# Optimization experiments

Measured on AMD Instinct MI355X. Metric: run time of the kernel, lower is better.

Reference implementation:

```python
import jax, jax.numpy as jnp
import numpy as np

K_PATCHES = 25
GRID_SIDE = 20            # sqrt(10000 // 25)
G = GRID_SIDE * GRID_SIDE # 400 points per patch
LATENT = 1024
DIMS = [LATENT + 2, 1024, 512, 256, 128, 3]  # per-layer in/out channels
BATCH = 16


def setup_inputs() -> dict:
    key = jax.random.key(0)
    ks = jax.random.split(key, 11)
    x = jax.random.normal(ks[0], (BATCH, LATENT), dtype=jnp.float32)
    params = {}
    # PyTorch Conv1d default init: U(-1/sqrt(fan_in), 1/sqrt(fan_in)); one weight set per patch.
    for i in range(5):
        fan_in = DIMS[i]
        bound = 1.0 / np.sqrt(fan_in)
        params[f"W{i+1}"] = jax.random.uniform(
            ks[1 + 2 * i], (K_PATCHES, DIMS[i], DIMS[i + 1]), jnp.float32, -bound, bound)
        params[f"b{i+1}"] = jax.random.uniform(
            ks[2 + 2 * i], (K_PATCHES, DIMS[i + 1]), jnp.float32, -bound, bound)
    return {"x": x, **params}


def reference(x, W1, b1, W2, b2, W3, b3, W4, b4, W5, b5):
    B = x.shape[0]
    # Deterministic UV grid (random_grid=False): same 20x20 grid for every patch.
    g = jnp.linspace(0.0, 1.0, GRID_SIDE)
    X, Y = jnp.meshgrid(g, g, indexing='xy')
    grid = jnp.stack([X, Y], axis=-1).reshape(-1, 2)  # (G, 2)
    # Build per-patch features: latent broadcast to every point + 2 uv coords.
    lat = jnp.broadcast_to(x[:, None, None, :], (B, K_PATCHES, G, LATENT))
    uv = jnp.broadcast_to(grid[None, None], (B, K_PATCHES, G, 2))
    h = jnp.concatenate([lat, uv], axis=-1)  # (B, P, G, 1026)
    # 1x1 Conv1d == per-point linear; batched over patches via grouped einsum.
    for W, b in ((W1, b1), (W2, b2), (W3, b3), (W4, b4)):
        h = jax.nn.relu(jnp.einsum('bpgi,pio->bpgo', h, W) + b[None, :, None, :])
    out = jnp.tanh(jnp.einsum('bpgi,pio->bpgo', h, W5) + b5[None, :, None, :])
    return out  # (B, P, G, 3) == torch stack(dim=1).permute(0,1,3,2)
```

## Files before the change

### kernel.cpp

```cpp
#include <hip/hip_runtime.h>
#include <math.h>

#define K_PATCHES 25
#define GRID_SIDE 20
#define G_PTS     400
#define LATENT    1024
#define BATCH     16

typedef _Float16 f16x8 __attribute__((ext_vector_type(8)));
typedef _Float16 f16x4 __attribute__((ext_vector_type(4)));
typedef float    f32x4 __attribute__((ext_vector_type(4)));

#define BASE_OFF 0
#define WT2_OFF  1638400
#define WT3_OFF  27852800
#define WT4_OFF  34406400

__global__ __launch_bounds__(128)
void base_kernel(const float* __restrict__ x,
                 const float* __restrict__ W1,
                 const float* __restrict__ b1,
                 float* __restrict__ base) {
    __shared__ float xs[BATCH][LATENT];
    const int p  = blockIdx.x >> 3;
    const int oc = blockIdx.x & 7;
    const int o  = oc * 128 + threadIdx.x;

    for (int idx = threadIdx.x; idx < BATCH * LATENT / 4; idx += 128)
        ((float4*)xs)[idx] = ((const float4*)x)[idx];
    __syncthreads();

    float acc[BATCH];
#pragma unroll
    for (int b = 0; b < BATCH; ++b) acc[b] = 0.0f;

    const float* Wp = W1 + (size_t)p * 1026 * 1024 + o;
    for (int k = 0; k < LATENT; k += 4) {
        const float w0 = Wp[(size_t)(k + 0) * 1024];
        const float w1 = Wp[(size_t)(k + 1) * 1024];
        const float w2 = Wp[(size_t)(k + 2) * 1024];
        const float w3 = Wp[(size_t)(k + 3) * 1024];
#pragma unroll
        for (int b = 0; b < BATCH; ++b) {
            const float4 xv = *(const float4*)&xs[b][k];
            acc[b] = fmaf(xv.w, w3, fmaf(xv.z, w2, fmaf(xv.y, w1, fmaf(xv.x, w0, acc[b]))));
        }
    }

    const float bias = b1[p * 1024 + o];
    for (int b = 0; b < BATCH; ++b)
        base[(size_t)(b * K_PATCHES + p) * 1024 + o] = acc[b] + bias;
}

__global__ __launch_bounds__(256)
void conv_tr_kernel(const float* __restrict__ W, _Float16* __restrict__ Wt,
                    int K, int N) {
    __shared__ float tile[64][65];
    const int tpp = (K / 64) * (N / 64);
    const int p   = blockIdx.x / tpp;
    const int rem = blockIdx.x % tpp;
    const int kt  = rem / (N / 64);
    const int nt  = rem % (N / 64);
    const int tr  = threadIdx.x >> 6;
    const int tc  = threadIdx.x & 63;

    const float* Wp = W + ((size_t)p * K + kt * 64) * N + nt * 64;
#pragma unroll
    for (int i = 0; i < 64; i += 4)
        tile[i + tr][tc] = Wp[(size_t)(i + tr) * N + tc];
    __syncthreads();

    _Float16* Wtp = Wt + ((size_t)p * N + nt * 64) * K + kt * 64;
#pragma unroll
    for (int i = 0; i < 64; i += 4)
        Wtp[(size_t)(i + tr) * K + tc] = (_Float16)tile[tc][i + tr];
}

__global__ __launch_bounds__(512)
void fused_mfma(const float* __restrict__ base,
                const float* __restrict__ W1,
                const _Float16* __restrict__ Wt2, const float* __restrict__ b2,
                const _Float16* __restrict__ Wt3, const float* __restrict__ b3,
                const _Float16* __restrict__ Wt4, const float* __restrict__ b4,
                const float* __restrict__ W5, const float* __restrict__ b5,
                float* __restrict__ out) {
    __shared__ __align__(16) unsigned char LDS[139264];
    constexpr int OFF_SB = 0;
    constexpr int OFF_WU = 8192;
    constexpr int OFF_WV = 12288;
    constexpr int OFF_H1 = 16384;
    constexpr int OFF_H2 = 24576;
    constexpr int OFF_H3 = 90112;
    constexpr int OFF_H4 = 122880;

    const int bid = blockIdx.x;
    const int xcd = bid & 7;
    const int ii  = bid >> 3;
    const int ord = (xcd < 4) ? xcd * 313 + ii : 4 * 313 + (xcd - 4) * 312 + ii;
    const int p     = ord / 100;
    const int rbase = (ord % 100) * 64;

    const int t    = threadIdx.x;
    const int lane = t & 63;
    const int w    = t >> 6;
    const int l16  = lane & 15;
    const int lq   = lane >> 4;

    float* sb0  = (float*)(LDS + OFF_SB);
    float* sb1  = sb0 + 1024;
    float* swuf = (float*)(LDS + OFF_WU);
    float* swvf = (float*)(LDS + OFF_WV);

    const int b0  = rbase / 400;
    const int b1i = (rbase + 63) / 400;
    {
        const float* base0 = base + (size_t)(b0 * K_PATCHES + p) * 1024;
        const float* base1 = base + (size_t)(b1i * K_PATCHES + p) * 1024;
        const float* wup   = W1 + (size_t)p * 1026 * 1024 + (size_t)1024 * 1024;
        if (t < 256) ((float4*)sb0)[t] = ((const float4*)base0)[t];
        else         ((float4*)sb1)[t - 256] = ((const float4*)base1)[t - 256];
        if (t < 256) ((float4*)swuf)[t] = ((const float4*)wup)[t];
        else         ((float4*)swvf)[t - 256] = ((const float4*)(wup + 1024))[t - 256];
    }
    __syncthreads();

    const int pko   = t >> 7;
    const int pr    = (t >> 1) & 63;
    const int phalf = t & 1;
    const float* sbm2 = (rbase + pr < (b0 + 1) * 400) ? sb0 : sb1;
    const int pg  = (rbase + pr) % 400;
    const float pu = (float)(pg % GRID_SIDE) * (1.0f / 19.0f);
    const float pv = (float)(pg / GRID_SIDE) * (1.0f / 19.0f);
    const unsigned pwoff = (unsigned)((pko * 64 + pr) * 16 + phalf * 8);

    auto produce2 = [&](int kc, unsigned char* dst) {
        const int k = kc + pko * 8 + phalf * 4;
        const float4 bv = *(const float4*)&sbm2[k];
        const float4 uu = *(const float4*)&swuf[k];
        const float4 vv = *(const float4*)&swvf[k];
        f16x4 hv;
        hv[0] = (_Float16)fmaxf(fmaf(pv, vv.x, fmaf(pu, uu.x, bv.x)), 0.0f);
        hv[1] = (_Float16)fmaxf(fmaf(pv, vv.y, fmaf(pu, uu.y, bv.y)), 0.0f);
        hv[2] = (_Float16)fmaxf(fmaf(pv, vv.z, fmaf(pu, uu.z, bv.z)), 0.0f);
        hv[3] = (_Float16)fmaxf(fmaf(pv, vv.w, fmaf(pu, uu.w, bv.w)), 0.0f);
        *(f16x4*)(dst + pwoff) = hv;
    };

    const _Float16* Wt2p = Wt2 + (size_t)p * 512 * 1024;
    const _Float16* b2base = Wt2p + (size_t)(w * 64 + l16) * 1024 + lq * 8;
    f32x4 acc2[4][4];
    {
        const float* b2p = b2 + p * 512;
#pragma unroll
        for (int nf = 0; nf < 4; ++nf) {
            const float bias = b2p[w * 64 + nf * 16 + l16];
            f32x4 bv = {bias, bias, bias, bias};
#pragma unroll
            for (int mf = 0; mf < 4; ++mf) acc2[mf][nf] = bv;
        }
    }

    f16x8 bA[4], bB[4];
    produce2(0, LDS + OFF_H1);
#pragma unroll
    for (int nf = 0; nf < 4; ++nf)
        bA[nf] = *(const f16x8*)(b2base + (size_t)nf * 16384);
    __syncthreads();

    auto l2step = [&](int c, f16x8 (&bc)[4], f16x8 (&bn)[4]) {
        const unsigned char* h1b = LDS + OFF_H1 + (c & 1) * 4096;
        if (c < 31) {
            const int kc1 = (c + 1) * 32;
#pragma unroll
            for (int nf = 0; nf < 4; ++nf)
                bn[nf] = *(const f16x8*)(b2base + (size_t)nf * 16384 + kc1);
            produce2(kc1, LDS + OFF_H1 + ((c + 1) & 1) * 4096);
        }
        f16x8 a[4];
#pragma unroll
        for (int mf = 0; mf < 4; ++mf)
            a[mf] = *(const f16x8*)(h1b + (lq * 64 + mf * 16 + l16) * 16);
        __builtin_amdgcn_s_setprio(1);
#pragma unroll
        for (int mf = 0; mf < 4; ++mf)
#pragma unroll
            for (int nf = 0; nf < 4; ++nf)
                acc2[mf][nf] = __builtin_amdgcn_mfma_f32_16x16x32_f16(a[mf], bc[nf], acc2[mf][nf], 0, 0, 0);
        __builtin_amdgcn_s_setprio(0);
        __syncthreads();
    };

#pragma unroll 1
    for (int c = 0; c < 32; c += 2) {
        l2step(c,     bA, bB);
        l2step(c + 1, bB, bA);
    }

#pragma unroll
    for (int mf = 0; mf < 4; ++mf)
#pragma unroll
        for (int nf = 0; nf < 4; ++nf)
#pragma unroll
            for (int r = 0; r < 4; ++r) {
                const int row = mf * 16 + lq * 4 + r;
                const int col = w * 64 + nf * 16 + l16;
                const float v = fmaxf(acc2[mf][nf][r], 0.0f);
                *(_Float16*)(LDS + OFF_H2 + ((col >> 3) * 64 + row) * 16 + (col & 7) * 2) = (_Float16)v;
            }
    __syncthreads();

    const _Float16* Wt3p = Wt3 + (size_t)p * 256 * 512;
    const _Float16* b3base = Wt3p + (size_t)(w * 32 + l16) * 512 + lq * 8;
    f32x4 acc3[4][2];
    {
        const float* b3p = b3 + p * 256;
#pragma unroll
        for (int nf = 0; nf < 2; ++nf) {
            const float bias = b3p[w * 32 + nf * 16 + l16];
            f32x4 bv = {bias, bias, bias, bias};
#pragma unroll
            for (int mf = 0; mf < 4; ++mf) acc3[mf][nf] = bv;
        }
    }
    f16x8 cA[2], cB[2];
#pragma unroll
    for (int nf = 0; nf < 2; ++nf)
        cA[nf] = *(const f16x8*)(b3base + (size_t)nf * 8192);

    auto l3step = [&](int c, f16x8 (&bc)[2], f16x8 (&bn)[2]) {
        if (c < 15) {
            const int kc1 = (c + 1) * 32;
#pragma unroll
            for (int nf = 0; nf < 2; ++nf)
                bn[nf] = *(const f16x8*)(b3base + (size_t)nf * 8192 + kc1);
        }
        f16x8 a[4];
#pragma unroll
        for (int mf = 0; mf < 4; ++mf)
            a[mf] = *(const f16x8*)(LDS + OFF_H2 + ((c * 4 + lq) * 64 + mf * 16 + l16) * 16);
        __builtin_amdgcn_s_setprio(1);
#pragma unroll
        for (int mf = 0; mf < 4; ++mf)
#pragma unroll
            for (int nf = 0; nf < 2; ++nf)
                acc3[mf][nf] = __builtin_amdgcn_mfma_f32_16x16x32_f16(a[mf], bc[nf], acc3[mf][nf], 0, 0, 0);
        __builtin_amdgcn_s_setprio(0);
    };

#pragma unroll 1
    for (int c = 0; c < 16; c += 2) {
        l3step(c,     cA, cB);
        l3step(c + 1, cB, cA);
    }

#pragma unroll
    for (int mf = 0; mf < 4; ++mf)
#pragma unroll
        for (int nf = 0; nf < 2; ++nf)
#pragma unroll
            for (int r = 0; r < 4; ++r) {
                const int row = mf * 16 + lq * 4 + r;
                const int col = w * 32 + nf * 16 + l16;
                const float v = fmaxf(acc3[mf][nf][r], 0.0f);
                *(_Float16*)(LDS + OFF_H3 + ((col >> 3) * 64 + row) * 16 + (col & 7) * 2) = (_Float16)v;
            }
    __syncthreads();

    const _Float16* Wt4p = Wt4 + (size_t)p * 128 * 256;
    const _Float16* b4base = Wt4p + (size_t)(w * 16 + l16) * 256 + lq * 8;
    f32x4 acc4[4];
    {
        const float* b4p = b4 + p * 128;
        const float bias = b4p[w * 16 + l16];
        f32x4 bv = {bias, bias, bias, bias};
#pragma unroll
        for (int mf = 0; mf < 4; ++mf) acc4[mf] = bv;
    }
    f16x8 dA, dB;
    dA = *(const f16x8*)(b4base);

    auto l4step = [&](int c, f16x8& bc, f16x8& bn) {
        if (c < 7)
            bn = *(const f16x8*)(b4base + (c + 1) * 32);
        f16x8 a[4];
#pragma unroll
        for (int mf = 0; mf < 4; ++mf)
            a[mf] = *(const f16x8*)(LDS + OFF_H3 + ((c * 4 + lq) * 64 + mf * 16 + l16) * 16);
        __builtin_amdgcn_s_setprio(1);
#pragma unroll
        for (int mf = 0; mf < 4; ++mf)
            acc4[mf] = __builtin_amdgcn_mfma_f32_16x16x32_f16(a[mf], bc, acc4[mf], 0, 0, 0);
        __builtin_amdgcn_s_setprio(0);
    };

#pragma unroll 1
    for (int c = 0; c < 8; c += 2) {
        l4step(c,     dA, dB);
        l4step(c + 1, dB, dA);
    }

#pragma unroll
    for (int mf = 0; mf < 4; ++mf)
#pragma unroll
        for (int r = 0; r < 4; ++r) {
            const int row = mf * 16 + lq * 4 + r;
            const int col = w * 16 + l16;
            const float v = fmaxf(acc4[mf][r], 0.0f);
            *(_Float16*)(LDS + OFF_H4 + ((col >> 3) * 64 + row) * 16 + (col & 7) * 2) = (_Float16)v;
        }
    __syncthreads();

    if (t < 192) {
        const int m = t / 3;
        const int c = t % 3;
        const float* W5p = W5 + p * 128 * 3;
        float acc = b5[p * 3 + c];
#pragma unroll 4
        for (int k = 0; k < 128; ++k) {
            const _Float16 hv = *(const _Float16*)(LDS + OFF_H4 + ((k >> 3) * 64 + m) * 16 + (k & 7) * 2);
            acc = fmaf((float)hv, W5p[k * 3 + c], acc);
        }
        const int r  = rbase + m;
        const int bb = r / 400;
        const int gg = r % 400;
        out[((size_t)(bb * K_PATCHES + p) * G_PTS + gg) * 3 + c] = tanhf(acc);
    }
}

extern "C" void kernel_launch(void* const* d_in, const int* in_sizes, int n_in,
                              void* d_out, int out_size, void* d_ws, size_t ws_size,
                              hipStream_t stream) {
    const float* x  = (const float*)d_in[0];
    const float* W1 = (const float*)d_in[1];
    const float* b1 = (const float*)d_in[2];
    const float* W2 = (const float*)d_in[3];
    const float* b2 = (const float*)d_in[4];
    const float* W3 = (const float*)d_in[5];
    const float* b3 = (const float*)d_in[6];
    const float* W4 = (const float*)d_in[7];
    const float* b4 = (const float*)d_in[8];
    const float* W5 = (const float*)d_in[9];
    const float* b5 = (const float*)d_in[10];
    float* out = (float*)d_out;

    float*     base = (float*)((char*)d_ws + BASE_OFF);
    _Float16*  Wt2  = (_Float16*)((char*)d_ws + WT2_OFF);
    _Float16*  Wt3  = (_Float16*)((char*)d_ws + WT3_OFF);
    _Float16*  Wt4  = (_Float16*)((char*)d_ws + WT4_OFF);

    base_kernel<<<K_PATCHES * 8, 128, 0, stream>>>(x, W1, b1, base);

    conv_tr_kernel<<<K_PATCHES * (1024 / 64) * (512 / 64), 256, 0, stream>>>(W2, Wt2, 1024, 512);
    conv_tr_kernel<<<K_PATCHES * (512 / 64) * (256 / 64),  256, 0, stream>>>(W3, Wt3, 512, 256);
    conv_tr_kernel<<<K_PATCHES * (256 / 64) * (128 / 64),  256, 0, stream>>>(W4, Wt4, 256, 128);

    fused_mfma<<<K_PATCHES * 100, 512, 0, stream>>>(
        base, W1, Wt2, b2, Wt3, b3, Wt4, b4, W5, b5, out);
}
```

Before: 594.5 us.

## Split fused MLP kernel into two lower-LDS kernels via fp16 workspace intermediate

The single fused kernel used about 136 KB of LDS per block, which limited occupancy. It is split into gemm_l12 (layers 1-2, writes h2 as fp16 to global workspace) and gemm_l345 (layers 3-5, reads h2 straight from global into registers). Each uses far less LDS and sets launch_bounds occupancy hints. The three weight-transpose launches are also merged into one. This costs an extra roundtrip of about 164 MB of fp16 activations through memory, and the split path only runs when the workspace is large enough, otherwise it falls back to the fused kernel.

Result: slower. 720.6 us (+21.2%).

```diff
diff --git a/kernel.cpp b/kernel.cpp
--- a/kernel.cpp
+++ b/kernel.cpp
@@ -15,6 +15,8 @@
 #define WT2_OFF  1638400
 #define WT3_OFF  27852800
 #define WT4_OFF  34406400
+#define H2WS_OFF 36044800
+#define WS_NEED  (36044800ull + 163840000ull)
 
 __global__ __launch_bounds__(128)
 void base_kernel(const float* __restrict__ x,
@@ -53,12 +55,19 @@
 }
 
 __global__ __launch_bounds__(256)
-void conv_tr_kernel(const float* __restrict__ W, _Float16* __restrict__ Wt,
-                    int K, int N) {
+void conv_tr_all(const float* __restrict__ W2, _Float16* __restrict__ Wt2,
+                 const float* __restrict__ W3, _Float16* __restrict__ Wt3,
+                 const float* __restrict__ W4, _Float16* __restrict__ Wt4) {
     __shared__ float tile[64][65];
+    int bb = blockIdx.x;
+    const float* W; _Float16* Wt; int K, N, rel;
+    if (bb < 3200)      { W = W2; Wt = Wt2; K = 1024; N = 512; rel = bb; }
+    else if (bb < 4000) { W = W3; Wt = Wt3; K = 512;  N = 256; rel = bb - 3200; }
+    else                { W = W4; Wt = Wt4; K = 256;  N = 128; rel = bb - 4000; }
+
     const int tpp = (K / 64) * (N / 64);
-    const int p   = blockIdx.x / tpp;
-    const int rem = blockIdx.x % tpp;
+    const int p   = rel / tpp;
+    const int rem = rel % tpp;
     const int kt  = rem / (N / 64);
     const int nt  = rem % (N / 64);
     const int tr  = threadIdx.x >> 6;
@@ -74,6 +83,280 @@
 #pragma unroll
     for (int i = 0; i < 64; i += 4)
         Wtp[(size_t)(i + tr) * K + tc] = (_Float16)tile[tc][i + tr];
+}
+
+__device__ __forceinline__ int tile_ord(int bid) {
+    const int xcd = bid & 7;
+    const int ii  = bid >> 3;
+    return (xcd < 4) ? xcd * 313 + ii : 4 * 313 + (xcd - 4) * 312 + ii;
+}
+
+__global__ __launch_bounds__(512, 4)
+void gemm_l12(const float* __restrict__ base,
+              const float* __restrict__ W1,
+              const _Float16* __restrict__ Wt2, const float* __restrict__ b2,
+              _Float16* __restrict__ h2g) {
+    __shared__ __align__(16) unsigned char LDS[24576];
+    constexpr int OFF_SB = 0;
+    constexpr int OFF_WU = 8192;
+    constexpr int OFF_WV = 12288;
+    constexpr int OFF_H1 = 16384;
+
+    const int ord   = tile_ord(blockIdx.x);
+    const int p     = ord / 100;
+    const int rbase = (ord % 100) * 64;
+
+    const int t    = threadIdx.x;
+    const int lane = t & 63;
+    const int w    = t >> 6;
+    const int l16  = lane & 15;
+    const int lq   = lane >> 4;
+
+    float* sb0  = (float*)(LDS + OFF_SB);
+    float* sb1  = sb0 + 1024;
+    float* swuf = (float*)(LDS + OFF_WU);
+    float* swvf = (float*)(LDS + OFF_WV);
+
+    const int b0  = rbase / 400;
+    const int b1i = (rbase + 63) / 400;
+    {
+        const float* base0 = base + (size_t)(b0 * K_PATCHES + p) * 1024;
+        const float* base1 = base + (size_t)(b1i * K_PATCHES + p) * 1024;
+        const float* wup   = W1 + (size_t)p * 1026 * 1024 + (size_t)1024 * 1024;
+        if (t < 256) ((float4*)sb0)[t] = ((const float4*)base0)[t];
+        else         ((float4*)sb1)[t - 256] = ((const float4*)base1)[t - 256];
+        if (t < 256) ((float4*)swuf)[t] = ((const float4*)wup)[t];
+        else         ((float4*)swvf)[t - 256] = ((const float4*)(wup + 1024))[t - 256];
+    }
+    __syncthreads();
+
+    const int pko   = t >> 7;
+    const int pr    = (t >> 1) & 63;
+    const int phalf = t & 1;
+    const float* sbm2 = (rbase + pr < (b0 + 1) * 400) ? sb0 : sb1;
+    const int pg  = (rbase + pr) % 400;
+    const float pu = (float)(pg % GRID_SIDE) * (1.0f / 19.0f);
+    const float pv = (float)(pg / GRID_SIDE) * (1.0f / 19.0f);
+    const unsigned pwoff = (unsigned)((pko * 64 + pr) * 16 + phalf * 8);
+
+    auto produce2 = [&](int kc, unsigned char* dst) {
+        const int k = kc + pko * 8 + phalf * 4;
+        const float4 bv = *(const float4*)&sbm2[k];
+        const float4 uu = *(const float4*)&swuf[k];
+        const float4 vv = *(const float4*)&swvf[k];
+        f16x4 hv;
+        hv[0] = (_Float16)fmaxf(fmaf(pv, vv.x, fmaf(pu, uu.x, bv.x)), 0.0f);
+        hv[1] = (_Float16)fmaxf(fmaf(pv, vv.y, fmaf(pu, uu.y, bv.y)), 0.0f);
+        hv[2] = (_Float16)fmaxf(fmaf(pv, vv.z, fmaf(pu, uu.z, bv.z)), 0.0f);
+        hv[3] = (_Float16)fmaxf(fmaf(pv, vv.w, fmaf(pu, uu.w, bv.w)), 0.0f);
+        *(f16x4*)(dst + pwoff) = hv;
+    };
+
+    const _Float16* Wt2p = Wt2 + (size_t)p * 512 * 1024;
+    const _Float16* b2base = Wt2p + (size_t)(w * 64 + l16) * 1024 + lq * 8;
+    f32x4 acc2[4][4];
+    {
+        const float* b2p = b2 + p * 512;
+#pragma unroll
+        for (int nf = 0; nf < 4; ++nf) {
+            const float bias = b2p[w * 64 + nf * 16 + l16];
+            f32x4 bv = {bias, bias, bias, bias};
+#pragma unroll
+            for (int mf = 0; mf < 4; ++mf) acc2[mf][nf] = bv;
+        }
+    }
+
+    f16x8 bA[4], bB[4];
+    produce2(0, LDS + OFF_H1);
+#pragma unroll
+    for (int nf = 0; nf < 4; ++nf)
+        bA[nf] = *(const f16x8*)(b2base + (size_t)nf * 16384);
+    __syncthreads();
+
+    auto l2step = [&](int c, f16x8 (&bc)[4], f16x8 (&bn)[4]) {
+        const unsigned char* h1b = LDS + OFF_H1 + (c & 1) * 4096;
+        if (c < 31) {
+            const int kc1 = (c + 1) * 32;
+#pragma unroll
+            for (int nf = 0; nf < 4; ++nf)
+                bn[nf] = *(const f16x8*)(b2base + (size_t)nf * 16384 + kc1);
+            produce2(kc1, LDS + OFF_H1 + ((c + 1) & 1) * 4096);
+        }
+        f16x8 a[4];
+#pragma unroll
+        for (int mf = 0; mf < 4; ++mf)
+            a[mf] = *(const f16x8*)(h1b + (lq * 64 + mf * 16 + l16) * 16);
+        __builtin_amdgcn_s_setprio(1);
+#pragma unroll
+        for (int mf = 0; mf < 4; ++mf)
+#pragma unroll
+            for (int nf = 0; nf < 4; ++nf)
+                acc2[mf][nf] = __builtin_amdgcn_mfma_f32_16x16x32_f16(a[mf], bc[nf], acc2[mf][nf], 0, 0, 0);
+        __builtin_amdgcn_s_setprio(0);
+        __syncthreads();
+    };
+
+#pragma unroll 1
+    for (int c = 0; c < 32; c += 2) {
+        l2step(c,     bA, bB);
+        l2step(c + 1, bB, bA);
+    }
+
+    _Float16* hp = h2g + (size_t)ord * 64 * 512;
+#pragma unroll
+    for (int mf = 0; mf < 4; ++mf)
+#pragma unroll
+        for (int nf = 0; nf < 4; ++nf)
+#pragma unroll
+            for (int r = 0; r < 4; ++r) {
+                const int row = mf * 16 + lq * 4 + r;
+                const int col = w * 64 + nf * 16 + l16;
+                hp[row * 512 + col] = (_Float16)fmaxf(acc2[mf][nf][r], 0.0f);
+            }
+}
+
+__global__ __launch_bounds__(512, 4)
+void gemm_l345(const _Float16* __restrict__ h2g,
+               const _Float16* __restrict__ Wt3, const float* __restrict__ b3,
+               const _Float16* __restrict__ Wt4, const float* __restrict__ b4,
+               const float* __restrict__ W5, const float* __restrict__ b5,
+               float* __restrict__ out) {
+    __shared__ __align__(16) unsigned char LDS[49152];
+    constexpr int OFF_H3 = 0;
+    constexpr int OFF_H4 = 32768;
+
+    const int ord   = tile_ord(blockIdx.x);
+    const int p     = ord / 100;
+    const int rbase = (ord % 100) * 64;
+
+    const int t    = threadIdx.x;
+    const int lane = t & 63;
+    const int w    = t >> 6;
+    const int l16  = lane & 15;
+    const int lq   = lane >> 4;
+
+    const _Float16* hp = h2g + (size_t)ord * 64 * 512;
+    const _Float16* a2base = hp + (size_t)l16 * 512 + lq * 8;
+
+    const _Float16* Wt3p = Wt3 + (size_t)p * 256 * 512;
+    const _Float16* b3base = Wt3p + (size_t)(w * 32 + l16) * 512 + lq * 8;
+    f32x4 acc3[4][2];
+    {
+        const float* b3p = b3 + p * 256;
+#pragma unroll
+        for (int nf = 0; nf < 2; ++nf) {
+            const float bias = b3p[w * 32 + nf * 16 + l16];
+            f32x4 bv = {bias, bias, bias, bias};
+#pragma unroll
+            for (int mf = 0; mf < 4; ++mf) acc3[mf][nf] = bv;
+        }
+    }
+    f16x8 aA[4], aB[4], cA[2], cB[2];
+#pragma unroll
+    for (int mf = 0; mf < 4; ++mf)
+        aA[mf] = *(const f16x8*)(a2base + (size_t)mf * 8192);
+#pragma unroll
+    for (int nf = 0; nf < 2; ++nf)
+        cA[nf] = *(const f16x8*)(b3base + (size_t)nf * 8192);
+
+    auto l3step = [&](int c, f16x8 (&ac)[4], f16x8 (&an)[4],
+                      f16x8 (&bc)[2], f16x8 (&bn)[2]) {
+        if (c < 15) {
+            const int kc1 = (c + 1) * 32;
+#pragma unroll
+            for (int mf = 0; mf < 4; ++mf)
+                an[mf] = *(const f16x8*)(a2base + (size_t)mf * 8192 + kc1);
+#pragma unroll
+            for (int nf = 0; nf < 2; ++nf)
+                bn[nf] = *(const f16x8*)(b3base + (size_t)nf * 8192 + kc1);
+        }
+        __builtin_amdgcn_s_setprio(1);
+#pragma unroll
+        for (int mf = 0; mf < 4; ++mf)
+#pragma unroll
+            for (int nf = 0; nf < 2; ++nf)
+                acc3[mf][nf] = __builtin_amdgcn_mfma_f32_16x16x32_f16(ac[mf], bc[nf], acc3[mf][nf], 0, 0, 0);
+        __builtin_amdgcn_s_setprio(0);
+    };
+
+#pragma unroll 1
+    for (int c = 0; c < 16; c += 2) {
+        l3step(c,     aA, aB, cA, cB);
+        l3step(c + 1, aB, aA, cB, cA);
+    }
+
+#pragma unroll
+    for (int mf = 0; mf < 4; ++mf)
+#pragma unroll
+        for (int nf = 0; nf < 2; ++nf)
+#pragma unroll
+            for (int r = 0; r < 4; ++r) {
+                const int row = mf * 16 + lq * 4 + r;
+                const int col = w * 32 + nf * 16 + l16;
+                const float v = fmaxf(acc3[mf][nf][r], 0.0f);
+                *(_Float16*)(LDS + OFF_H3 + ((col >> 3) * 64 + row) * 16 + (col & 7) * 2) = (_Float16)v;
+            }
+    __syncthreads();
+
+    const _Float16* Wt4p = Wt4 + (size_t)p * 128 * 256;
+    const _Float16* b4base = Wt4p + (size_t)(w * 16 + l16) * 256 + lq * 8;
+    f32x4 acc4[4];
+    {
+        const float* b4p = b4 + p * 128;
+        const float bias = b4p[w * 16 + l16];
+        f32x4 bv = {bias, bias, bias, bias};
+#pragma unroll
+        for (int mf = 0; mf < 4; ++mf) acc4[mf] = bv;
+    }
+    f16x8 dA, dB;
+    dA = *(const f16x8*)(b4base);
+
+    auto l4step = [&](int c, f16x8& bc, f16x8& bn) {
+        if (c < 7)
+            bn = *(const f16x8*)(b4base + (c + 1) * 32);
+        f16x8 a[4];
+#pragma unroll
+        for (int mf = 0; mf < 4; ++mf)
+            a[mf] = *(const f16x8*)(LDS + OFF_H3 + ((c * 4 + lq) * 64 + mf * 16 + l16) * 16);
+        __builtin_amdgcn_s_setprio(1);
+#pragma unroll
+        for (int mf = 0; mf < 4; ++mf)
+            acc4[mf] = __builtin_amdgcn_mfma_f32_16x16x32_f16(a[mf], bc, acc4[mf], 0, 0, 0);
+        __builtin_amdgcn_s_setprio(0);
+    };
+
+#pragma unroll 1
+    for (int c = 0; c < 8; c += 2) {
+        l4step(c,     dA, dB);
+        l4step(c + 1, dB, dA);
+    }
+
+#pragma unroll
+    for (int mf = 0; mf < 4; ++mf)
+#pragma unroll
+        for (int r = 0; r < 4; ++r) {
+            const int row = mf * 16 + lq * 4 + r;
+            const int col = w * 16 + l16;
+            const float v = fmaxf(acc4[mf][r], 0.0f);
+            *(_Float16*)(LDS + OFF_H4 + ((col >> 3) * 64 + row) * 16 + (col & 7) * 2) = (_Float16)v;
+        }
+    __syncthreads();
+
+    if (t < 192) {
+        const int m = t / 3;
+        const int c = t % 3;
+        const float* W5p = W5 + p * 128 * 3;
+        float acc = b5[p * 3 + c];
+#pragma unroll 4
+        for (int k = 0; k < 128; ++k) {
+            const _Float16 hv = *(const _Float16*)(LDS + OFF_H4 + ((k >> 3) * 64 + m) * 16 + (k & 7) * 2);
+            acc = fmaf((float)hv, W5p[k * 3 + c], acc);
+        }
+        const int r  = rbase + m;
+        const int bb = r / 400;
+        const int gg = r % 400;
+        out[((size_t)(bb * K_PATCHES + p) * G_PTS + gg) * 3 + c] = tanhf(acc);
+    }
 }
 
 __global__ __launch_bounds__(512)
@@ -93,10 +376,7 @@
     constexpr int OFF_H3 = 90112;
     constexpr int OFF_H4 = 122880;
 
-    const int bid = blockIdx.x;
-    const int xcd = bid & 7;
-    const int ii  = bid >> 3;
-    const int ord = (xcd < 4) ? xcd * 313 + ii : 4 * 313 + (xcd - 4) * 312 + ii;
+    const int ord   = tile_ord(blockIdx.x);
     const int p     = ord / 100;
     const int rbase = (ord % 100) * 64;
 
@@ -347,13 +627,16 @@
     _Float16*  Wt2  = (_Float16*)((char*)d_ws + WT2_OFF);
     _Float16*  Wt3  = (_Float16*)((char*)d_ws + WT3_OFF);
     _Float16*  Wt4  = (_Float16*)((char*)d_ws + WT4_OFF);
+    _Float16*  h2g  = (_Float16*)((char*)d_ws + H2WS_OFF);
 
     base_kernel<<<K_PATCHES * 8, 128, 0, stream>>>(x, W1, b1, base);
-
-    conv_tr_kernel<<<K_PATCHES * (1024 / 64) * (512 / 64), 256, 0, stream>>>(W2, Wt2, 1024, 512);
-    conv_tr_kernel<<<K_PATCHES * (512 / 64) * (256 / 64),  256, 0, stream>>>(W3, Wt3, 512, 256);
-    conv_tr_kernel<<<K_PATCHES * (256 / 64) * (128 / 64),  256, 0, stream>>>(W4, Wt4, 256, 128);
-
-    fused_mfma<<<K_PATCHES * 100, 512, 0, stream>>>(
-        base, W1, Wt2, b2, Wt3, b3, Wt4, b4, W5, b5, out);
+    conv_tr_all<<<4200, 256, 0, stream>>>(W2, Wt2, W3, Wt3, W4, Wt4);
+
+    if (ws_size >= WS_NEED) {
+        gemm_l12<<<K_PATCHES * 100, 512, 0, stream>>>(base, W1, Wt2, b2, h2g);
+        gemm_l345<<<K_PATCHES * 100, 512, 0, stream>>>(h2g, Wt3, b3, Wt4, b4, W5, b5, out);
+    } else {
+        fused_mfma<<<K_PATCHES * 100, 512, 0, stream>>>(
+            base, W1, Wt2, b2, Wt3, b3, Wt4, b4, W5, b5, out);
+    }
 }
```

## Split fused MLP into layer-1/2 and layer-3/4/5 kernels with 128-row tiles

Applied to the files above, without the earlier changes.

The single fused kernel is split in two. The first computes layers 1-2 with 128x256 tiles and writes the layer-2 activations to a global workspace in fp16. The second computes layers 3-5 on 128-row tiles, reading those activations straight from global into registers, and uses a waitcnt-plus-barrier macro in place of __syncthreads. The three transpose launches are also merged into one. The aim is to lower LDS use so more blocks fit per CU, and to double the row tile so weights are reused more; the cost is a global round-trip of the hidden activations and an extra launch.

Result: slower. 641.9 us (+8.0%).

```diff
diff --git a/kernel.cpp b/kernel.cpp
--- a/kernel.cpp
+++ b/kernel.cpp
@@ -8,13 +8,20 @@
 #define BATCH     16
 
 typedef _Float16 f16x8 __attribute__((ext_vector_type(8)));
-typedef _Float16 f16x4 __attribute__((ext_vector_type(4)));
 typedef float    f32x4 __attribute__((ext_vector_type(4)));
+
+#define LGKM_BAR() do {                                      \
+    asm volatile("s_waitcnt lgkmcnt(0)" ::: "memory");       \
+    __builtin_amdgcn_sched_barrier(0);                       \
+    __builtin_amdgcn_s_barrier();                            \
+    __builtin_amdgcn_sched_barrier(0);                       \
+} while (0)
 
 #define BASE_OFF 0
 #define WT2_OFF  1638400
 #define WT3_OFF  27852800
 #define WT4_OFF  34406400
+#define H2WS_OFF 36044800
 
 __global__ __launch_bounds__(128)
 void base_kernel(const float* __restrict__ x,
@@ -53,12 +60,19 @@
 }
 
 __global__ __launch_bounds__(256)
-void conv_tr_kernel(const float* __restrict__ W, _Float16* __restrict__ Wt,
-                    int K, int N) {
+void conv_tr_all(const float* __restrict__ W2, _Float16* __restrict__ Wt2,
+                 const float* __restrict__ W3, _Float16* __restrict__ Wt3,
+                 const float* __restrict__ W4, _Float16* __restrict__ Wt4) {
     __shared__ float tile[64][65];
+    int bb = blockIdx.x;
+    const float* W; _Float16* Wt; int K, N, rel;
+    if (bb < 3200)      { W = W2; Wt = Wt2; K = 1024; N = 512; rel = bb; }
+    else if (bb < 4000) { W = W3; Wt = Wt3; K = 512;  N = 256; rel = bb - 3200; }
+    else                { W = W4; Wt = Wt4; K = 256;  N = 128; rel = bb - 4000; }
+
     const int tpp = (K / 64) * (N / 64);
-    const int p   = blockIdx.x / tpp;
-    const int rem = blockIdx.x % tpp;
+    const int p   = rel / tpp;
+    const int rem = rel % tpp;
     const int kt  = rem / (N / 64);
     const int nt  = rem % (N / 64);
     const int tr  = threadIdx.x >> 6;
@@ -76,33 +90,40 @@
         Wtp[(size_t)(i + tr) * K + tc] = (_Float16)tile[tc][i + tr];
 }
 
+__device__ __forceinline__ int tile_ord2500(int bid) {
+    const int xcd = bid & 7;
+    const int ii  = bid >> 3;
+    return (xcd < 4) ? xcd * 313 + ii : 4 * 313 + (xcd - 4) * 312 + ii;
+}
+__device__ __forceinline__ int tile_ord1250(int bid) {
+    const int xcd = bid & 7;
+    const int ii  = bid >> 3;
+    return (xcd < 2) ? xcd * 157 + ii : 2 * 157 + (xcd - 2) * 156 + ii;
+}
+
 __global__ __launch_bounds__(512)
-void fused_mfma(const float* __restrict__ base,
-                const float* __restrict__ W1,
-                const _Float16* __restrict__ Wt2, const float* __restrict__ b2,
-                const _Float16* __restrict__ Wt3, const float* __restrict__ b3,
-                const _Float16* __restrict__ Wt4, const float* __restrict__ b4,
-                const float* __restrict__ W5, const float* __restrict__ b5,
-                float* __restrict__ out) {
-    __shared__ __align__(16) unsigned char LDS[139264];
+void gemm_l12(const float* __restrict__ base,
+              const float* __restrict__ W1,
+              const _Float16* __restrict__ Wt2, const float* __restrict__ b2,
+              _Float16* __restrict__ h2g) {
+    __shared__ __align__(16) unsigned char LDS[32768];
     constexpr int OFF_SB = 0;
     constexpr int OFF_WU = 8192;
     constexpr int OFF_WV = 12288;
     constexpr int OFF_H1 = 16384;
-    constexpr int OFF_H2 = 24576;
-    constexpr int OFF_H3 = 90112;
-    constexpr int OFF_H4 = 122880;
-
-    const int bid = blockIdx.x;
-    const int xcd = bid & 7;
-    const int ii  = bid >> 3;
-    const int ord = (xcd < 4) ? xcd * 313 + ii : 4 * 313 + (xcd - 4) * 312 + ii;
-    const int p     = ord / 100;
-    const int rbase = (ord % 100) * 64;
+
+    const int ord = tile_ord2500(blockIdx.x);
+    const int p   = ord / 100;
+    const int rem = ord % 100;
+    const int mt  = rem >> 1;
+    const int nh  = rem & 1;
+    const int rbase = mt * 128;
 
     const int t    = threadIdx.x;
     const int lane = t & 63;
     const int w    = t >> 6;
+    const int wm   = w >> 2;
+    const int wn   = w & 3;
     const int l16  = lane & 15;
     const int lq   = lane >> 4;
 
@@ -111,10 +132,10 @@
     float* swuf = (float*)(LDS + OFF_WU);
     float* swvf = (float*)(LDS + OFF_WV);
 
-    const int b0  = rbase / 400;
-    const int b1i = (rbase + 63) / 400;
+    const int b0i = rbase / 400;
+    const int b1i = (rbase + 127) / 400;
     {
-        const float* base0 = base + (size_t)(b0 * K_PATCHES + p) * 1024;
+        const float* base0 = base + (size_t)(b0i * K_PATCHES + p) * 1024;
         const float* base1 = base + (size_t)(b1i * K_PATCHES + p) * 1024;
         const float* wup   = W1 + (size_t)p * 1026 * 1024 + (size_t)1024 * 1024;
         if (t < 256) ((float4*)sb0)[t] = ((const float4*)base0)[t];
@@ -124,62 +145,65 @@
     }
     __syncthreads();
 
-    const int pko   = t >> 7;
-    const int pr    = (t >> 1) & 63;
-    const int phalf = t & 1;
-    const float* sbm2 = (rbase + pr < (b0 + 1) * 400) ? sb0 : sb1;
+    const int pr = t & 127;
+    const int pq = t >> 7;
+    const float* sbm2 = (rbase + pr < (b0i + 1) * 400) ? sb0 : sb1;
     const int pg  = (rbase + pr) % 400;
     const float pu = (float)(pg % GRID_SIDE) * (1.0f / 19.0f);
     const float pv = (float)(pg / GRID_SIDE) * (1.0f / 19.0f);
-    const unsigned pwoff = (unsigned)((pko * 64 + pr) * 16 + phalf * 8);
+    const unsigned pwoff = (unsigned)((pq * 128 + pr) * 16);
 
     auto produce2 = [&](int kc, unsigned char* dst) {
-        const int k = kc + pko * 8 + phalf * 4;
-        const float4 bv = *(const float4*)&sbm2[k];
-        const float4 uu = *(const float4*)&swuf[k];
-        const float4 vv = *(const float4*)&swvf[k];
-        f16x4 hv;
-        hv[0] = (_Float16)fmaxf(fmaf(pv, vv.x, fmaf(pu, uu.x, bv.x)), 0.0f);
-        hv[1] = (_Float16)fmaxf(fmaf(pv, vv.y, fmaf(pu, uu.y, bv.y)), 0.0f);
-        hv[2] = (_Float16)fmaxf(fmaf(pv, vv.z, fmaf(pu, uu.z, bv.z)), 0.0f);
-        hv[3] = (_Float16)fmaxf(fmaf(pv, vv.w, fmaf(pu, uu.w, bv.w)), 0.0f);
-        *(f16x4*)(dst + pwoff) = hv;
+        const int k = kc + pq * 8;
+        const float4 bv0 = *(const float4*)&sbm2[k];
+        const float4 bv1 = *(const float4*)&sbm2[k + 4];
+        const float4 u0  = *(const float4*)&swuf[k];
+        const float4 u1  = *(const float4*)&swuf[k + 4];
+        const float4 v0  = *(const float4*)&swvf[k];
+        const float4 v1  = *(const float4*)&swvf[k + 4];
+        f16x8 hv;
+        hv[0] = (_Float16)fmaxf(fmaf(pv, v0.x, fmaf(pu, u0.x, bv0.x)), 0.0f);
+        hv[1] = (_Float16)fmaxf(fmaf(pv, v0.y, fmaf(pu, u0.y, bv0.y)), 0.0f);
+        hv[2] = (_Float16)fmaxf(fmaf(pv, v0.z, fmaf(pu, u0.z, bv0.z)), 0.0f);
+        hv[3] = (_Float16)fmaxf(fmaf(pv, v0.w, fmaf(pu, u0.w, bv0.w)), 0.0f);
+        hv[4] = (_Float16)fmaxf(fmaf(pv, v1.x, fmaf(pu, u1.x, bv1.x)), 0.0f);
+        hv[5] = (_Float16)fmaxf(fmaf(pv, v1.y, fmaf(pu, u1.y, bv1.y)), 0.0f);
+        hv[6] = (_Float16)fmaxf(fmaf(pv, v1.z, fmaf(pu, u1.z, bv1.z)), 0.0f);
+        hv[7] = (_Float16)fmaxf(fmaf(pv, v1.w, fmaf(pu, u1.w, bv1.w)), 0.0f);
+        *(f16x8*)(dst + pwoff) = hv;
     };
 
     const _Float16* Wt2p = Wt2 + (size_t)p * 512 * 1024;
-    const _Float16* b2base = Wt2p + (size_t)(w * 64 + l16) * 1024 + lq * 8;
+    const _Float16* b2base = Wt2p + (size_t)(nh * 256 + wn * 64 + l16) * 1024 + lq * 8;
     f32x4 acc2[4][4];
     {
         const float* b2p = b2 + p * 512;
 #pragma unroll
         for (int nf = 0; nf < 4; ++nf) {
-            const float bias = b2p[w * 64 + nf * 16 + l16];
+            const float bias = b2p[nh * 256 + wn * 64 + nf * 16 + l16];
             f32x4 bv = {bias, bias, bias, bias};
 #pragma unroll
             for (int mf = 0; mf < 4; ++mf) acc2[mf][nf] = bv;
         }
     }
 
-    f16x8 bA[4], bB[4];
+    f16x8 bX[4], bY[4];
     produce2(0, LDS + OFF_H1);
 #pragma unroll
-    for (int nf = 0; nf < 4; ++nf)
-        bA[nf] = *(const f16x8*)(b2base + (size_t)nf * 16384);
+    for (int nf = 0; nf < 4; ++nf) {
+        bX[nf] = *(const f16x8*)(b2base + (size_t)nf * 16384);
+        bY[nf] = *(const f16x8*)(b2base + (size_t)nf * 16384 + 32);
+    }
     __syncthreads();
 
-    auto l2step = [&](int c, f16x8 (&bc)[4], f16x8 (&bn)[4]) {
-        const unsigned char* h1b = LDS + OFF_H1 + (c & 1) * 4096;
-        if (c < 31) {
-            const int kc1 = (c + 1) * 32;
-#pragma unroll
-            for (int nf = 0; nf < 4; ++nf)
-                bn[nf] = *(const f16x8*)(b2base + (size_t)nf * 16384 + kc1);
-            produce2(kc1, LDS + OFF_H1 + ((c + 1) & 1) * 4096);
-        }
+    auto l2chunk = [&](int c, f16x8 (&bc)[4]) {
+        const unsigned char* h1b = LDS + OFF_H1 + (c & 1) * 8192;
         f16x8 a[4];
 #pragma unroll
         for (int mf = 0; mf < 4; ++mf)
-            a[mf] = *(const f16x8*)(h1b + (lq * 64 + mf * 16 + l16) * 16);
+            a[mf] = *(const f16x8*)(h1b + (lq * 128 + wm * 64 + mf * 16 + l16) * 16);
+        if (c + 1 < 32)
+            produce2((c + 1) * 32, LDS + OFF_H1 + ((c + 1) & 1) * 8192);
         __builtin_amdgcn_s_setprio(1);
 #pragma unroll
         for (int mf = 0; mf < 4; ++mf)
@@ -187,137 +211,175 @@
             for (int nf = 0; nf < 4; ++nf)
                 acc2[mf][nf] = __builtin_amdgcn_mfma_f32_16x16x32_f16(a[mf], bc[nf], acc2[mf][nf], 0, 0, 0);
         __builtin_amdgcn_s_setprio(0);
-        __syncthreads();
+        if (c + 2 < 32) {
+            const int kc2 = (c + 2) * 32;
+#pragma unroll
+            for (int nf = 0; nf < 4; ++nf)
+                bc[nf] = *(const f16x8*)(b2base + (size_t)nf * 16384 + kc2);
+        }
+        LGKM_BAR();
     };
 
 #pragma unroll 1
     for (int c = 0; c < 32; c += 2) {
-        l2step(c,     bA, bB);
-        l2step(c + 1, bB, bA);
-    }
-
+        l2chunk(c,     bX);
+        l2chunk(c + 1, bY);
+    }
+
+    _Float16* hp = h2g + (size_t)(p * 50 + mt) * 128 * 512;
 #pragma unroll
     for (int mf = 0; mf < 4; ++mf)
 #pragma unroll
         for (int nf = 0; nf < 4; ++nf)
 #pragma unroll
             for (int r = 0; r < 4; ++r) {
-                const int row = mf * 16 + lq * 4 + r;
-                const int col = w * 64 + nf * 16 + l16;
-                const float v = fmaxf(acc2[mf][nf][r], 0.0f);
-                *(_Float16*)(LDS + OFF_H2 + ((col >> 3) * 64 + row) * 16 + (col & 7) * 2) = (_Float16)v;
+                const int row = wm * 64 + mf * 16 + lq * 4 + r;
+                const int col = nh * 256 + wn * 64 + nf * 16 + l16;
+                hp[(size_t)(col >> 3) * 1024 + row * 8 + (col & 7)] =
+                    (_Float16)fmaxf(acc2[mf][nf][r], 0.0f);
             }
-    __syncthreads();
+}
+
+__global__ __launch_bounds__(512)
+void gemm_l345(const _Float16* __restrict__ h2g,
+               const _Float16* __restrict__ Wt3, const float* __restrict__ b3,
+               const _Float16* __restrict__ Wt4, const float* __restrict__ b4,
+               const float* __restrict__ W5, const float* __restrict__ b5,
+               float* __restrict__ out) {
+    __shared__ __align__(16) unsigned char LDS[98304];
+    constexpr int OFF_H3 = 0;
+    constexpr int OFF_H4 = 65536;
+
+    const int ord   = tile_ord1250(blockIdx.x);
+    const int p     = ord / 50;
+    const int mt    = ord % 50;
+    const int rbase = mt * 128;
+
+    const int t    = threadIdx.x;
+    const int lane = t & 63;
+    const int w    = t >> 6;
+    const int wm   = w >> 2;
+    const int wn   = w & 3;
+    const int l16  = lane & 15;
+    const int lq   = lane >> 4;
+
+    const _Float16* hp = h2g + (size_t)ord * 128 * 512;
 
     const _Float16* Wt3p = Wt3 + (size_t)p * 256 * 512;
-    const _Float16* b3base = Wt3p + (size_t)(w * 32 + l16) * 512 + lq * 8;
-    f32x4 acc3[4][2];
+    const _Float16* b3base = Wt3p + (size_t)(wn * 64 + l16) * 512 + lq * 8;
+    f32x4 acc3[4][4];
     {
         const float* b3p = b3 + p * 256;
 #pragma unroll
-        for (int nf = 0; nf < 2; ++nf) {
-            const float bias = b3p[w * 32 + nf * 16 + l16];
+        for (int nf = 0; nf < 4; ++nf) {
+            const float bias = b3p[wn * 64 + nf * 16 + l16];
             f32x4 bv = {bias, bias, bias, bias};
 #pragma unroll
             for (int mf = 0; mf < 4; ++mf) acc3[mf][nf] = bv;
         }
     }
-    f16x8 cA[2], cB[2];
-#pragma unroll
-    for (int nf = 0; nf < 2; ++nf)
-        cA[nf] = *(const f16x8*)(b3base + (size_t)nf * 8192);
-
-    auto l3step = [&](int c, f16x8 (&bc)[2], f16x8 (&bn)[2]) {
-        if (c < 15) {
-            const int kc1 = (c + 1) * 32;
-#pragma unroll
-            for (int nf = 0; nf < 2; ++nf)
-                bn[nf] = *(const f16x8*)(b3base + (size_t)nf * 8192 + kc1);
-        }
-        f16x8 a[4];
+    const _Float16* a3base = hp + (size_t)(lq * 128 + wm * 64 + l16) * 8;
+
+    f16x8 aX[4], aY[4], cX[4], cY[4];
+#pragma unroll
+    for (int mf = 0; mf < 4; ++mf) {
+        aX[mf] = *(const f16x8*)(a3base + (size_t)mf * 128);
+        aY[mf] = *(const f16x8*)(a3base + (size_t)(4 * 1024 + mf * 128));
+    }
+#pragma unroll
+    for (int nf = 0; nf < 4; ++nf) {
+        cX[nf] = *(const f16x8*)(b3base + (size_t)nf * 8192);
+        cY[nf] = *(const f16x8*)(b3base + (size_t)nf * 8192 + 32);
+    }
+
+    auto l3chunk = [&](int c, f16x8 (&ac)[4], f16x8 (&bc)[4]) {
+        __builtin_amdgcn_s_setprio(1);
 #pragma unroll
         for (int mf = 0; mf < 4; ++mf)
-            a[mf] = *(const f16x8*)(LDS + OFF_H2 + ((c * 4 + lq) * 64 + mf * 16 + l16) * 16);
-        __builtin_amdgcn_s_setprio(1);
-#pragma unroll
-        for (int mf = 0; mf < 4; ++mf)
-#pragma unroll
-            for (int nf = 0; nf < 2; ++nf)
-                acc3[mf][nf] = __builtin_amdgcn_mfma_f32_16x16x32_f16(a[mf], bc[nf], acc3[mf][nf], 0, 0, 0);
+#pragma unroll
+            for (int nf = 0; nf < 4; ++nf)
+                acc3[mf][nf] = __builtin_amdgcn_mfma_f32_16x16x32_f16(ac[mf], bc[nf], acc3[mf][nf], 0, 0, 0);
         __builtin_amdgcn_s_setprio(0);
+        if (c + 2 < 16) {
+            const int kc2 = (c + 2) * 32;
+#pragma unroll
+            for (int mf = 0; mf < 4; ++mf)
+                ac[mf] = *(const f16x8*)(a3base + (size_t)((c + 2) * 4 * 1024 + mf * 128));
+#pragma unroll
+            for (int nf = 0; nf < 4; ++nf)
+                bc[nf] = *(const f16x8*)(b3base + (size_t)nf * 8192 + kc2);
+        }
     };
 
 #pragma unroll 1
     for (int c = 0; c < 16; c += 2) {
-        l3step(c,     cA, cB);
-        l3step(c + 1, cB, cA);
+        l3chunk(c,     aX, cX);
+        l3chunk(c + 1, aY, cY);
     }
 
 #pragma unroll
     for (int mf = 0; mf < 4; ++mf)
 #pragma unroll
-        for (int nf = 0; nf < 2; ++nf)
+        for (int nf = 0; nf < 4; ++nf)
 #pragma unroll
             for (int r = 0; r < 4; ++r) {
-                const int row = mf * 16 + lq * 4 + r;
-                const int col = w * 32 + nf * 16 + l16;
+                const int row = wm * 64 + mf * 16 + lq * 4 + r;
+                const int col = wn * 64 + nf * 16 + l16;
                 const float v = fmaxf(acc3[mf][nf][r], 0.0f);
-                *(_Float16*)(LDS + OFF_H3 + ((col >> 3) * 64 + row) * 16 + (col & 7) * 2) = (_Float16)v;
+                *(_Float16*)(LDS + OFF_H3 + ((col >> 3) * 128 + row) * 16 + (col & 7) * 2) = (_Float16)v;
             }
-    __syncthreads();
+    LGKM_BAR();
 
     const _Float16* Wt4p = Wt4 + (size_t)p * 128 * 256;
     const _Float16* b4base = Wt4p + (size_t)(w * 16 + l16) * 256 + lq * 8;
-    f32x4 acc4[4];
-    {
-        const float* b4p = b4 + p * 128;
-        const float bias = b4p[w * 16 + l16];
-        f32x4 bv = {bias, bias, bias, bias};
-#pragma unroll
-        for (int mf = 0; mf < 4; ++mf) acc4[mf] = bv;
-    }
-    f16x8 dA, dB;
-    dA = *(const f16x8*)(b4base);
-
-    auto l4step = [&](int c, f16x8& bc, f16x8& bn) {
-        if (c < 7)
-            bn = *(const f16x8*)(b4base + (c + 1) * 32);
-        f16x8 a[4];
+    f16x8 dreg[8];
+#pragma unroll
+    for (int c = 0; c < 8; ++c)
+        dreg[c] = *(const f16x8*)(b4base + c * 32);
+
+#pragma unroll 1
+    for (int half = 0; half < 2; ++half) {
+        f32x4 acc4[4];
+        {
+            const float* b4p = b4 + p * 128;
+            const float bias = b4p[w * 16 + l16];
+            f32x4 bv = {bias, bias, bias, bias};
+#pragma unroll
+            for (int mf = 0; mf < 4; ++mf) acc4[mf] = bv;
+        }
+#pragma unroll
+        for (int c = 0; c < 8; ++c) {
+            f16x8 a[4];
+#pragma unroll
+            for (int mf = 0; mf < 4; ++mf)
+                a[mf] = *(const f16x8*)(LDS + OFF_H3 +
+                         ((c * 4 + lq) * 128 + half * 64 + mf * 16 + l16) * 16);
+            __builtin_amdgcn_s_setprio(1);
+#pragma unroll
+            for (int mf = 0; mf < 4; ++mf)
+                acc4[mf] = __builtin_amdgcn_mfma_f32_16x16x32_f16(a[mf], dreg[c], acc4[mf], 0, 0, 0);
+            __builtin_amdgcn_s_setprio(0);
+        }
 #pragma unroll
         for (int mf = 0; mf < 4; ++mf)
-            a[mf] = *(const f16x8*)(LDS + OFF_H3 + ((c * 4 + lq) * 64 + mf * 16 + l16) * 16);
-        __builtin_amdgcn_s_setprio(1);
-#pragma unroll
-        for (int mf = 0; mf < 4; ++mf)
-            acc4[mf] = __builtin_amdgcn_mfma_f32_16x16x32_f16(a[mf], bc, acc4[mf], 0, 0, 0);
-        __builtin_amdgcn_s_setprio(0);
-    };
-
-#pragma unroll 1
-    for (int c = 0; c < 8; c += 2) {
-        l4step(c,     dA, dB);
-        l4step(c + 1, dB, dA);
-    }
-
-#pragma unroll
-    for (int mf = 0; mf < 4; ++mf)
-#pragma unroll
-        for (int r = 0; r < 4; ++r) {
-            const int row = mf * 16 + lq * 4 + r;
-            const int col = w * 16 + l16;
-            const float v = fmaxf(acc4[mf][r], 0.0f);
-            *(_Float16*)(LDS + OFF_H4 + ((col >> 3) * 64 + row) * 16 + (col & 7) * 2) = (_Float16)v;
-        }
-    __syncthreads();
-
-    if (t < 192) {
+#pragma unroll
+            for (int r = 0; r < 4; ++r) {
+                const int row = half * 64 + mf * 16 + lq * 4 + r;
+                const int col = w * 16 + l16;
+                const float v = fmaxf(acc4[mf][r], 0.0f);
+                *(_Float16*)(LDS + OFF_H4 + ((col >> 3) * 128 + row) * 16 + (col & 7) * 2) = (_Float16)v;
+            }
+    }
+    LGKM_BAR();
+
+    if (t < 384) {
         const int m = t / 3;
         const int c = t % 3;
         const float* W5p = W5 + p * 128 * 3;
         float acc = b5[p * 3 + c];
 #pragma unroll 4
         for (int k = 0; k < 128; ++k) {
-            const _Float16 hv = *(const _Float16*)(LDS + OFF_H4 + ((k >> 3) * 64 + m) * 16 + (k & 7) * 2);
+            const _Float16 hv = *(const _Float16*)(LDS + OFF_H4 + ((k >> 3) * 128 + m) * 16 + (k & 7) * 2);
             acc = fmaf((float)hv, W5p[k * 3 + c], acc);
         }
         const int r  = rbase + m;
@@ -347,13 +409,11 @@
     _Float16*  Wt2  = (_Float16*)((char*)d_ws + WT2_OFF);
     _Float16*  Wt3  = (_Float16*)((char*)d_ws + WT3_OFF);
     _Float16*  Wt4  = (_Float16*)((char*)d_ws + WT4_OFF);
+    _Float16*  h2g  = (_Float16*)((char*)d_ws + H2WS_OFF);
 
     base_kernel<<<K_PATCHES * 8, 128, 0, stream>>>(x, W1, b1, base);
-
-    conv_tr_kernel<<<K_PATCHES * (1024 / 64) * (512 / 64), 256, 0, stream>>>(W2, Wt2, 1024, 512);
-    conv_tr_kernel<<<K_PATCHES * (512 / 64) * (256 / 64),  256, 0, stream>>>(W3, Wt3, 512, 256);
-    conv_tr_kernel<<<K_PATCHES * (256 / 64) * (128 / 64),  256, 0, stream>>>(W4, Wt4, 256, 128);
-
-    fused_mfma<<<K_PATCHES * 100, 512, 0, stream>>>(
-        base, W1, Wt2, b2, Wt3, b3, Wt4, b4, W5, b5, out);
-}
+    conv_tr_all<<<4200, 256, 0, stream>>>(W2, Wt2, W3, Wt3, W4, Wt4);
+
+    gemm_l12<<<K_PATCHES * 100, 512, 0, stream>>>(base, W1, Wt2, b2, h2g);
+    gemm_l345<<<K_PATCHES * 50, 512, 0, stream>>>(h2g, Wt3, b3, Wt4, b4, W5, b5, out);
+}
```
